# Optimization experiments

Hardware: AMD Instinct MI355X
Metric: run time of the kernel (lower is better)

The kernel has to match this reference:

```python
import jax, jax.numpy as jnp
import numpy as np

N_NODES = 50000


def _gcn_norm(edge_index, n):
    # Add self-loops (PyG GCNConv default) and compute symmetric normalization.
    src = jnp.concatenate([edge_index[0], jnp.arange(n, dtype=edge_index.dtype)])
    dst = jnp.concatenate([edge_index[1], jnp.arange(n, dtype=edge_index.dtype)])
    deg = jax.ops.segment_sum(jnp.ones(src.shape[0], dtype=jnp.float32), dst,
                              num_segments=n)
    dinv = jnp.where(deg > 0, jax.lax.rsqrt(deg), 0.0)
    norm = dinv[src] * dinv[dst]  # [E+N]
    return src, dst, norm


def _gcn_conv(x, src, dst, norm, W, b, n):
    h = x @ W                              # [N, out] linear transform first
    msgs = h[src] * norm[:, None]          # gather + edge-wise scale [E+N, out]
    out = jax.ops.segment_sum(msgs, dst, num_segments=n)  # scatter-add
    return out + b


def setup_inputs() -> dict:
    key = jax.random.key(0)
    k1, k2, k3, k4 = jax.random.split(key, 4)
    N, E, F, H, C = N_NODES, 1600000, 128, 128, 64
    x = jax.random.normal(k1, (N, F), dtype=jnp.float32)
    edge_index = jax.random.randint(k2, (2, E), 0, N, dtype=jnp.int64)
    W1 = jax.random.normal(k3, (F, H), dtype=jnp.float32) * 0.05
    b1 = jnp.zeros((H,), dtype=jnp.float32)
    W2 = jax.random.normal(k4, (H, C), dtype=jnp.float32) * 0.05
    b2 = jnp.zeros((C,), dtype=jnp.float32)
    return {"x": x, "edge_index": edge_index, "W1": W1, "b1": b1,
            "W2": W2, "b2": b2}


def reference(x, edge_index, W1, b1, W2, b2):
    n = x.shape[0]
    src, dst, norm = _gcn_norm(edge_index, n)
    h = _gcn_conv(x, src, dst, norm, W1, b1, n)
    h = jax.nn.relu(h)
    out = _gcn_conv(h, src, dst, norm, W2, b2, n)
    return out
```

## Files before the change

### kernel.cpp

```cpp
#include <hip/hip_runtime.h>
#include <hip/hip_bf16.h>
#include <stdint.h>

#define N_NODES 50000
#define N_EDGES 1600000
#define N_TOT   (N_EDGES + N_NODES)
#define NBKT      256
#define BKT_NODES 196
#define BKT_CAP   7168
#define TILE      4096
#define EPT       16

typedef unsigned short u16;
typedef __attribute__((ext_vector_type(8))) short short8;
typedef __attribute__((ext_vector_type(4))) float floatx4;

__device__ __forceinline__ float b2f(u16 u) {
    union { unsigned int i; float f; } v; v.i = ((unsigned int)u) << 16; return v.f;
}
__device__ __forceinline__ float asf(unsigned u) {
    union { unsigned int i; float f; } v; v.i = u; return v.f;
}
__device__ __forceinline__ u16 f2b(float f) {
    union { unsigned int i; float f; } v; v.f = f;
    unsigned int r = (v.i + 0x7FFFu + ((v.i >> 16) & 1u)) >> 16;
    return (u16)r;
}

__global__ void k_detect(const unsigned* __restrict__ xw,
                         const unsigned* __restrict__ ew,
                         int* __restrict__ flags,
                         int* __restrict__ bktcnt) {
    __shared__ int cnt[2];
    int tid = threadIdx.x;
    bktcnt[tid] = 0;
    if (tid < 2) cnt[tid] = 0;
    __syncthreads();
    unsigned w = xw[tid];
    int e = (w >> 7) & 0xFF;
    int plaus = (e == 0) || (e >= 0x60 && e <= 0x9F);
    unsigned hw = ew[2 * tid + 1];
    atomicAdd(&cnt[0], plaus);
    atomicAdd(&cnt[1], hw == 0 ? 1 : 0);
    __syncthreads();
    if (tid == 0) {
        flags[0] = (cnt[0] < 160) ? 1 : 0;
        flags[1] = (cnt[1] > 250) ? 1 : 0;
    }
}

__global__ __launch_bounds__(256) void k_part(const int* __restrict__ ei,
                                              const int* __restrict__ flags,
                                              unsigned* __restrict__ pairs,
                                              int* __restrict__ bktcnt) {
    __shared__ unsigned pairsL[TILE];
    __shared__ unsigned char bktL[TILE];
    __shared__ int hist[NBKT], incl[NBKT], delta[NBKT];
    int tid = threadIdx.x;
    long base = (long)blockIdx.x * TILE;
    int i64 = flags[1];
    hist[tid] = 0;
    __syncthreads();

    int myb[EPT], myrank[EPT]; unsigned myp[EPT];
#pragma unroll
    for (int t = 0; t < EPT; t++) {
        long idx = base + t * 256 + tid;
        int b = -1; unsigned p = 0;
        if (idx < N_TOT) {
            int s, d;
            if (idx < N_EDGES) {
                if (i64) { s = ei[2 * idx]; d = ei[2 * (N_EDGES + idx)]; }
                else     { s = ei[idx];     d = ei[N_EDGES + idx]; }
            } else {
                s = d = (int)(idx - N_EDGES);
            }
            b = d / BKT_NODES;
            p = (unsigned)s | ((unsigned)(d - b * BKT_NODES) << 16);
        }
        myb[t] = b; myp[t] = p;
        myrank[t] = (b >= 0) ? atomicAdd(&hist[b], 1) : 0;
    }
    __syncthreads();

    int tot = hist[tid];
    incl[tid] = tot;
    __syncthreads();
    for (int o = 1; o < NBKT; o <<= 1) {
        int t2 = (tid >= o) ? incl[tid - o] : 0;
        __syncthreads();
        incl[tid] += t2;
        __syncthreads();
    }
    int excl = incl[tid] - tot;
    int gb = atomicAdd(&bktcnt[tid], tot);
    hist[tid]  = excl;
    delta[tid] = tid * BKT_CAP + gb - excl;
    __syncthreads();

#pragma unroll
    for (int t = 0; t < EPT; t++) {
        if (myb[t] >= 0) {
            int slot = hist[myb[t]] + myrank[t];
            pairsL[slot] = myp[t];
            bktL[slot]   = (unsigned char)myb[t];
        }
    }
    __syncthreads();
    int count = incl[NBKT - 1];
    for (int i = tid; i < count; i += 256) {
        int b = bktL[i];
        int pos = delta[b] + i;
        if (pos - b * BKT_CAP < BKT_CAP)
            pairs[pos] = pairsL[i];
    }
}

__global__ __launch_bounds__(256) void k_bktscan(const int* __restrict__ bktcnt,
                                                 int* __restrict__ bktbase) {
    __shared__ int s[NBKT];
    int tid = threadIdx.x;
    int v = bktcnt[tid];
    s[tid] = v;
    __syncthreads();
    for (int o = 1; o < NBKT; o <<= 1) {
        int t = (tid >= o) ? s[tid - o] : 0;
        __syncthreads();
        s[tid] += t;
        __syncthreads();
    }
    bktbase[tid] = s[tid] - v;
}

__global__ __launch_bounds__(256) void k_bucket(const unsigned* __restrict__ pairs,
                                                const int* __restrict__ bktcnt,
                                                const int* __restrict__ bktbase,
                                                int* __restrict__ rowstart,
                                                int* __restrict__ deg,
                                                float* __restrict__ dinv,
                                                u16* __restrict__ csr) {
    __shared__ u16 csrL[BKT_CAP];
    __shared__ int degL[NBKT], curL[NBKT], scanT[NBKT];
    int b = blockIdx.x, tid = threadIdx.x;
    int cnt  = bktcnt[b];
    int base = bktbase[b];
    const unsigned* reg = pairs + (size_t)b * BKT_CAP;
    degL[tid] = 0;
    __syncthreads();
    for (int i = tid; i < cnt; i += 256)
        atomicAdd(&degL[reg[i] >> 16], 1);
    __syncthreads();
    int v = degL[tid];
    scanT[tid] = v;
    __syncthreads();
    for (int o = 1; o < NBKT; o <<= 1) {
        int t = (tid >= o) ? scanT[tid - o] : 0;
        __syncthreads();
        scanT[tid] += t;
        __syncthreads();
    }
    int excl = scanT[tid] - v;
    curL[tid] = excl;
    int n = b * BKT_NODES + tid;
    if (tid < BKT_NODES && n < N_NODES) {
        rowstart[n] = base + excl;
        deg[n]      = v;
        dinv[n]     = rsqrtf((float)v);
    }
    __syncthreads();
    for (int i = tid; i < cnt; i += 256) {
        unsigned p = reg[i];
        int slot = atomicAdd(&curL[p >> 16], 1);
        csrL[slot] = (u16)(p & 0xFFFFu);
    }
    __syncthreads();
    for (int i = tid; i < cnt; i += 256)
        csr[base + i] = csrL[i];
}

template<int NOUT, bool ADYN>
__global__ __launch_bounds__(256) void k_gemm(const void* __restrict__ A,
                                              const void* __restrict__ W,
                                              const float* __restrict__ dinv,
                                              u16* __restrict__ out, int M,
                                              const int* __restrict__ flags) {
    const int isf32 = flags[0];
    constexpr int LDW = 136;
    __shared__ __align__(16) u16 Wt[NOUT * LDW];
    int tid = threadIdx.x;
    const float* Wf = (const float*)W;
    const u16*   Wu = (const u16*)W;
    for (int idx = tid; idx < 128 * NOUT; idx += 256) {
        int k = idx / NOUT, n = idx % NOUT;
        Wt[n * LDW + k] = isf32 ? f2b(Wf[idx]) : Wu[idx];
    }
    __syncthreads();

    int wave = tid >> 6, lane = tid & 63;
    int quad = lane >> 4, l16 = lane & 15;
    int r0 = blockIdx.x * 64 + wave * 16;
    int r = r0 + l16; if (r >= M) r = M - 1;

    floatx4 acc[NOUT / 16];
#pragma unroll
    for (int i = 0; i < NOUT / 16; i++) acc[i] = (floatx4)(0.f);

#pragma unroll
    for (int ks = 0; ks < 4; ks++) {
        short8 a;
        if (ADYN && isf32) {
            const float* af = (const float*)A + (size_t)r * 128 + ks * 32 + quad * 8;
            float4 v0 = ((const float4*)af)[0];
            float4 v1 = ((const float4*)af)[1];
            a[0] = (short)f2b(v0.x); a[1] = (short)f2b(v0.y);
            a[2] = (short)f2b(v0.z); a[3] = (short)f2b(v0.w);
            a[4] = (short)f2b(v1.x); a[5] = (short)f2b(v1.y);
            a[6] = (short)f2b(v1.z); a[7] = (short)f2b(v1.w);
        } else {
            a = ((const short8*)((const u16*)A + (size_t)r * 128))[ks * 4 + quad];
        }
#pragma unroll
        for (int nt = 0; nt < NOUT / 16; nt++) {
            const short8* bp = (const short8*)&Wt[(nt * 16 + l16) * LDW + ks * 32 + quad * 8];
            acc[nt] = __builtin_amdgcn_mfma_f32_16x16x32_bf16(a, *bp, acc[nt], 0, 0, 0);
        }
    }
    float sc[4];
#pragma unroll
    for (int j = 0; j < 4; j++) {
        int row = r0 + quad * 4 + j;
        sc[j] = dinv[row < M ? row : 0];
    }
#pragma unroll
    for (int nt = 0; nt < NOUT / 16; nt++) {
#pragma unroll
        for (int j = 0; j < 4; j++) {
            int row = r0 + quad * 4 + j;
            if (row < M) out[(size_t)row * NOUT + nt * 16 + l16] = f2b(acc[nt][j] * sc[j]);
        }
    }
}

#define ACCU(u, j) { acc[j].x += asf((u) << 16); acc[j].y += asf((u) & 0xFFFF0000u); }

__global__ __launch_bounds__(256) void k_agg1(const u16* __restrict__ h,
                                              const u16* __restrict__ csr,
                                              const int* __restrict__ rowstart,
                                              const int* __restrict__ deg,
                                              const float* __restrict__ dinv,
                                              const void* __restrict__ bias,
                                              u16* __restrict__ out,
                                              const int* __restrict__ flags) {
    int wave = threadIdx.x >> 6, lane = threadIdx.x & 63;
    int d = blockIdx.x * 4 + wave;
    if (d >= N_NODES) return;
    int oct = lane >> 3, l8 = lane & 7;
    int start = rowstart[d], end = start + deg[d];
    float2 acc[8];
#pragma unroll
    for (int j = 0; j < 8; j++) acc[j] = make_float2(0.f, 0.f);

    int e = start + oct;
    for (; e + 24 < end; e += 32) {
        int s0 = csr[e], s1 = csr[e + 8], s2 = csr[e + 16], s3 = csr[e + 24];
        const uint4* p0 = (const uint4*)(h + (size_t)s0 * 128) + l8 * 2;
        const uint4* p1 = (const uint4*)(h + (size_t)s1 * 128) + l8 * 2;
        const uint4* p2 = (const uint4*)(h + (size_t)s2 * 128) + l8 * 2;
        const uint4* p3 = (const uint4*)(h + (size_t)s3 * 128) + l8 * 2;
        uint4 a0 = p0[0], b0 = p0[1];
        uint4 a1 = p1[0], b1 = p1[1];
        uint4 a2 = p2[0], b2 = p2[1];
        uint4 a3 = p3[0], b3 = p3[1];
        ACCU(a0.x,0) ACCU(a0.y,1) ACCU(a0.z,2) ACCU(a0.w,3)
        ACCU(b0.x,4) ACCU(b0.y,5) ACCU(b0.z,6) ACCU(b0.w,7)
        ACCU(a1.x,0) ACCU(a1.y,1) ACCU(a1.z,2) ACCU(a1.w,3)
        ACCU(b1.x,4) ACCU(b1.y,5) ACCU(b1.z,6) ACCU(b1.w,7)
        ACCU(a2.x,0) ACCU(a2.y,1) ACCU(a2.z,2) ACCU(a2.w,3)
        ACCU(b2.x,4) ACCU(b2.y,5) ACCU(b2.z,6) ACCU(b2.w,7)
        ACCU(a3.x,0) ACCU(a3.y,1) ACCU(a3.z,2) ACCU(a3.w,3)
        ACCU(b3.x,4) ACCU(b3.y,5) ACCU(b3.z,6) ACCU(b3.w,7)
    }
    for (; e < end; e += 8) {
        int s0 = csr[e];
        const uint4* p0 = (const uint4*)(h + (size_t)s0 * 128) + l8 * 2;
        uint4 a0 = p0[0], b0 = p0[1];
        ACCU(a0.x,0) ACCU(a0.y,1) ACCU(a0.z,2) ACCU(a0.w,3)
        ACCU(b0.x,4) ACCU(b0.y,5) ACCU(b0.z,6) ACCU(b0.w,7)
    }
#pragma unroll
    for (int j = 0; j < 8; j++) {
        acc[j].x += __shfl_xor(acc[j].x, 8);  acc[j].y += __shfl_xor(acc[j].y, 8);
        acc[j].x += __shfl_xor(acc[j].x, 16); acc[j].y += __shfl_xor(acc[j].y, 16);
        acc[j].x += __shfl_xor(acc[j].x, 32); acc[j].y += __shfl_xor(acc[j].y, 32);
    }
    if (oct == 0) {
        int isf32 = flags[0];
        float dd = dinv[d];
        u16 r[16];
#pragma unroll
        for (int j = 0; j < 8; j++) {
            float bx = isf32 ? ((const float*)bias)[l8 * 16 + 2 * j]
                             : b2f(((const u16*)bias)[l8 * 16 + 2 * j]);
            float by = isf32 ? ((const float*)bias)[l8 * 16 + 2 * j + 1]
                             : b2f(((const u16*)bias)[l8 * 16 + 2 * j + 1]);
            float vx = acc[j].x * dd + bx;
            float vy = acc[j].y * dd + by;
            r[2 * j]     = f2b(vx > 0.f ? vx : 0.f);
            r[2 * j + 1] = f2b(vy > 0.f ? vy : 0.f);
        }
        uint4 o0, o1;
        o0.x = r[0] | ((unsigned)r[1] << 16);  o0.y = r[2] | ((unsigned)r[3] << 16);
        o0.z = r[4] | ((unsigned)r[5] << 16);  o0.w = r[6] | ((unsigned)r[7] << 16);
        o1.x = r[8] | ((unsigned)r[9] << 16);  o1.y = r[10] | ((unsigned)r[11] << 16);
        o1.z = r[12] | ((unsigned)r[13] << 16); o1.w = r[14] | ((unsigned)r[15] << 16);
        ((uint4*)(out + (size_t)d * 128))[l8 * 2]     = o0;
        ((uint4*)(out + (size_t)d * 128))[l8 * 2 + 1] = o1;
    }
}

__global__ __launch_bounds__(256) void k_agg2(const u16* __restrict__ h,
                                              const u16* __restrict__ csr,
                                              const int* __restrict__ rowstart,
                                              const int* __restrict__ deg,
                                              const float* __restrict__ dinv,
                                              const void* __restrict__ bias,
                                              float* __restrict__ out,
                                              const int* __restrict__ flags) {
    int wave = threadIdx.x >> 6, lane = threadIdx.x & 63;
    int d = blockIdx.x * 4 + wave;
    if (d >= N_NODES) return;
    int oct = lane >> 3, l8 = lane & 7;
    int start = rowstart[d], end = start + deg[d];
    float2 acc[4];
#pragma unroll
    for (int j = 0; j < 4; j++) acc[j] = make_float2(0.f, 0.f);

    int e = start + oct;
    for (; e + 24 < end; e += 32) {
        int s0 = csr[e], s1 = csr[e + 8], s2 = csr[e + 16], s3 = csr[e + 24];
        uint4 v0 = ((const uint4*)(h + (size_t)s0 * 64))[l8];
        uint4 v1 = ((const uint4*)(h + (size_t)s1 * 64))[l8];
        uint4 v2 = ((const uint4*)(h + (size_t)s2 * 64))[l8];
        uint4 v3 = ((const uint4*)(h + (size_t)s3 * 64))[l8];
        ACCU(v0.x,0) ACCU(v0.y,1) ACCU(v0.z,2) ACCU(v0.w,3)
        ACCU(v1.x,0) ACCU(v1.y,1) ACCU(v1.z,2) ACCU(v1.w,3)
        ACCU(v2.x,0) ACCU(v2.y,1) ACCU(v2.z,2) ACCU(v2.w,3)
        ACCU(v3.x,0) ACCU(v3.y,1) ACCU(v3.z,2) ACCU(v3.w,3)
    }
    for (; e < end; e += 8) {
        int s0 = csr[e];
        uint4 v0 = ((const uint4*)(h + (size_t)s0 * 64))[l8];
        ACCU(v0.x,0) ACCU(v0.y,1) ACCU(v0.z,2) ACCU(v0.w,3)
    }
#pragma unroll
    for (int j = 0; j < 4; j++) {
        acc[j].x += __shfl_xor(acc[j].x, 8);  acc[j].y += __shfl_xor(acc[j].y, 8);
        acc[j].x += __shfl_xor(acc[j].x, 16); acc[j].y += __shfl_xor(acc[j].y, 16);
        acc[j].x += __shfl_xor(acc[j].x, 32); acc[j].y += __shfl_xor(acc[j].y, 32);
    }
    if (oct == 0) {
        int isf32 = flags[0];
        float dd = dinv[d];
        float r[8];
#pragma unroll
        for (int j = 0; j < 4; j++) {
            float bx = isf32 ? ((const float*)bias)[l8 * 8 + 2 * j]
                             : b2f(((const u16*)bias)[l8 * 8 + 2 * j]);
            float by = isf32 ? ((const float*)bias)[l8 * 8 + 2 * j + 1]
                             : b2f(((const u16*)bias)[l8 * 8 + 2 * j + 1]);
            r[2 * j]     = acc[j].x * dd + bx;
            r[2 * j + 1] = acc[j].y * dd + by;
        }
        float4* op = (float4*)(out + (size_t)d * 64) + l8 * 2;
        op[0] = make_float4(r[0], r[1], r[2], r[3]);
        op[1] = make_float4(r[4], r[5], r[6], r[7]);
    }
}

extern "C" void kernel_launch(void* const* d_in, const int* in_sizes, int n_in,
                              void* d_out, int out_size, void* d_ws, size_t ws_size,
                              hipStream_t stream) {
    const void* x  = d_in[0];
    const int*  ei = (const int*)d_in[1];
    const void* W1 = d_in[2];
    const void* b1 = d_in[3];
    const void* W2 = d_in[4];
    const void* b2 = d_in[5];
    float* out = (float*)d_out;

    char* ws = (char*)d_ws;
    int*      flags    = (int*)(ws + 0);
    int*      bktcnt   = (int*)(ws + 1024);
    int*      bktbase  = (int*)(ws + 2048);
    int*      deg      = (int*)(ws + 4096);
    int*      rowstart = (int*)(ws + 204800);
    float*    dinv     = (float*)(ws + 405504);
    unsigned* pairs    = (unsigned*)(ws + 606208);
    u16*      csr      = (u16*)(ws + 7946240);
    u16*      h1       = (u16*)(ws + 11247616);
    u16*      out1     = (u16*)(ws + 24047616);
    u16*      h2       = h1;

    k_detect <<<1, 256, 0, stream>>>((const unsigned*)x, (const unsigned*)ei, flags, bktcnt);
    k_part   <<<(N_TOT + TILE - 1) / TILE, 256, 0, stream>>>(ei, flags, pairs, bktcnt);
    k_bktscan<<<1, 256, 0, stream>>>(bktcnt, bktbase);
    k_bucket <<<NBKT, 256, 0, stream>>>(pairs, bktcnt, bktbase, rowstart, deg, dinv, csr);

    k_gemm<128, true> <<<(N_NODES + 63) / 64, 256, 0, stream>>>(x, W1, dinv, h1, N_NODES, flags);
    k_agg1<<<(N_NODES + 3) / 4, 256, 0, stream>>>(h1, csr, rowstart, deg, dinv, b1, out1, flags);
    k_gemm<64, false> <<<(N_NODES + 63) / 64, 256, 0, stream>>>(out1, W2, dinv, h2, N_NODES, flags);
    k_agg2<<<(N_NODES + 3) / 4, 256, 0, stream>>>(h2, csr, rowstart, deg, dinv, b2, out, flags);
}
```

Measured before the change: 255.6 us.

## Store hidden features in 32-column panels and aggregate one panel per block

The GEMM now writes its bf16 output in panel-major layout (32 features per panel, plus a zero pad row per panel), and the aggregation kernels launch one grid slice per panel so each gather reads a 64-byte panel row. The goal is a smaller working set per pass, so the gathered features stay resident in cache across random neighbor accesses. The inner loop is also reworked to process 16 edges per step with masked tails that point at the zero pad row, replacing the separate remainder loop. In exchange, edge indices and degrees are read once per panel, and h2 is moved to reuse the pairs buffer region.

```diff
diff --git a/kernel.cpp b/kernel.cpp
--- a/kernel.cpp
+++ b/kernel.cpp
@@ -10,6 +10,8 @@
 #define BKT_CAP   7168
 #define TILE      4096
 #define EPT       16
+#define NGRP      12500
+#define PROWS     (N_NODES + 1)
 
 typedef unsigned short u16;
 typedef __attribute__((ext_vector_type(8))) short short8;
@@ -188,6 +190,8 @@
     constexpr int LDW = 136;
     __shared__ __align__(16) u16 Wt[NOUT * LDW];
     int tid = threadIdx.x;
+    if (blockIdx.x == 0 && tid < NOUT)
+        out[((size_t)((tid >> 5) * PROWS) + N_NODES) * 32 + (tid & 31)] = 0;
     const float* Wf = (const float*)W;
     const u16*   Wu = (const u16*)W;
     for (int idx = tid; idx < 128 * NOUT; idx += 256) {
@@ -233,10 +237,13 @@
     }
 #pragma unroll
     for (int nt = 0; nt < NOUT / 16; nt++) {
+        int col = nt * 16 + l16;
+        int p = col >> 5, c = col & 31;
 #pragma unroll
         for (int j = 0; j < 4; j++) {
             int row = r0 + quad * 4 + j;
-            if (row < M) out[(size_t)row * NOUT + nt * 16 + l16] = f2b(acc[nt][j] * sc[j]);
+            if (row < M)
+                out[((size_t)(p * PROWS) + row) * 32 + c] = f2b(acc[nt][j] * sc[j]);
         }
     }
 }
@@ -252,69 +259,55 @@
                                               u16* __restrict__ out,
                                               const int* __restrict__ flags) {
     int wave = threadIdx.x >> 6, lane = threadIdx.x & 63;
-    int d = blockIdx.x * 4 + wave;
-    if (d >= N_NODES) return;
-    int oct = lane >> 3, l8 = lane & 7;
-    int start = rowstart[d], end = start + deg[d];
-    float2 acc[8];
-#pragma unroll
-    for (int j = 0; j < 8; j++) acc[j] = make_float2(0.f, 0.f);
-
-    int e = start + oct;
-    for (; e + 24 < end; e += 32) {
-        int s0 = csr[e], s1 = csr[e + 8], s2 = csr[e + 16], s3 = csr[e + 24];
-        const uint4* p0 = (const uint4*)(h + (size_t)s0 * 128) + l8 * 2;
-        const uint4* p1 = (const uint4*)(h + (size_t)s1 * 128) + l8 * 2;
-        const uint4* p2 = (const uint4*)(h + (size_t)s2 * 128) + l8 * 2;
-        const uint4* p3 = (const uint4*)(h + (size_t)s3 * 128) + l8 * 2;
-        uint4 a0 = p0[0], b0 = p0[1];
-        uint4 a1 = p1[0], b1 = p1[1];
-        uint4 a2 = p2[0], b2 = p2[1];
-        uint4 a3 = p3[0], b3 = p3[1];
-        ACCU(a0.x,0) ACCU(a0.y,1) ACCU(a0.z,2) ACCU(a0.w,3)
-        ACCU(b0.x,4) ACCU(b0.y,5) ACCU(b0.z,6) ACCU(b0.w,7)
-        ACCU(a1.x,0) ACCU(a1.y,1) ACCU(a1.z,2) ACCU(a1.w,3)
-        ACCU(b1.x,4) ACCU(b1.y,5) ACCU(b1.z,6) ACCU(b1.w,7)
-        ACCU(a2.x,0) ACCU(a2.y,1) ACCU(a2.z,2) ACCU(a2.w,3)
-        ACCU(b2.x,4) ACCU(b2.y,5) ACCU(b2.z,6) ACCU(b2.w,7)
-        ACCU(a3.x,0) ACCU(a3.y,1) ACCU(a3.z,2) ACCU(a3.w,3)
-        ACCU(b3.x,4) ACCU(b3.y,5) ACCU(b3.z,6) ACCU(b3.w,7)
-    }
-    for (; e < end; e += 8) {
-        int s0 = csr[e];
-        const uint4* p0 = (const uint4*)(h + (size_t)s0 * 128) + l8 * 2;
-        uint4 a0 = p0[0], b0 = p0[1];
-        ACCU(a0.x,0) ACCU(a0.y,1) ACCU(a0.z,2) ACCU(a0.w,3)
-        ACCU(b0.x,4) ACCU(b0.y,5) ACCU(b0.z,6) ACCU(b0.w,7)
-    }
-#pragma unroll
-    for (int j = 0; j < 8; j++) {
+    int gb = blockIdx.x % NGRP, panel = blockIdx.x / NGRP;
+    int d = gb * 4 + wave;
+    int grp = lane >> 2, l4 = lane & 3;
+    int start = rowstart[d], dg = deg[d], end = start + dg;
+    const u16* hp = h + (size_t)(panel * PROWS) * 32;
+    float2 acc[4];
+#pragma unroll
+    for (int j = 0; j < 4; j++) acc[j] = make_float2(0.f, 0.f);
+
+    int rounds = (dg + 31) >> 5;
+    int e = start + grp;
+    for (int r = 0; r < rounds; r++, e += 32) {
+        int e1 = e + 16;
+        int s0 = csr[e  < end ? e  : start];
+        int s1 = csr[e1 < end ? e1 : start];
+        s0 = (e  < end) ? s0 : N_NODES;
+        s1 = (e1 < end) ? s1 : N_NODES;
+        uint4 v0 = ((const uint4*)(hp + (size_t)s0 * 32))[l4];
+        uint4 v1 = ((const uint4*)(hp + (size_t)s1 * 32))[l4];
+        ACCU(v0.x,0) ACCU(v0.y,1) ACCU(v0.z,2) ACCU(v0.w,3)
+        ACCU(v1.x,0) ACCU(v1.y,1) ACCU(v1.z,2) ACCU(v1.w,3)
+    }
+#pragma unroll
+    for (int j = 0; j < 4; j++) {
+        acc[j].x += __shfl_xor(acc[j].x, 4);  acc[j].y += __shfl_xor(acc[j].y, 4);
         acc[j].x += __shfl_xor(acc[j].x, 8);  acc[j].y += __shfl_xor(acc[j].y, 8);
         acc[j].x += __shfl_xor(acc[j].x, 16); acc[j].y += __shfl_xor(acc[j].y, 16);
         acc[j].x += __shfl_xor(acc[j].x, 32); acc[j].y += __shfl_xor(acc[j].y, 32);
     }
-    if (oct == 0) {
+    if (grp == 0) {
         int isf32 = flags[0];
         float dd = dinv[d];
-        u16 r[16];
-#pragma unroll
-        for (int j = 0; j < 8; j++) {
-            float bx = isf32 ? ((const float*)bias)[l8 * 16 + 2 * j]
-                             : b2f(((const u16*)bias)[l8 * 16 + 2 * j]);
-            float by = isf32 ? ((const float*)bias)[l8 * 16 + 2 * j + 1]
-                             : b2f(((const u16*)bias)[l8 * 16 + 2 * j + 1]);
+        int fb = panel * 32 + l4 * 8;
+        u16 r[8];
+#pragma unroll
+        for (int j = 0; j < 4; j++) {
+            float bx = isf32 ? ((const float*)bias)[fb + 2 * j]
+                             : b2f(((const u16*)bias)[fb + 2 * j]);
+            float by = isf32 ? ((const float*)bias)[fb + 2 * j + 1]
+                             : b2f(((const u16*)bias)[fb + 2 * j + 1]);
             float vx = acc[j].x * dd + bx;
             float vy = acc[j].y * dd + by;
             r[2 * j]     = f2b(vx > 0.f ? vx : 0.f);
             r[2 * j + 1] = f2b(vy > 0.f ? vy : 0.f);
         }
-        uint4 o0, o1;
-        o0.x = r[0] | ((unsigned)r[1] << 16);  o0.y = r[2] | ((unsigned)r[3] << 16);
-        o0.z = r[4] | ((unsigned)r[5] << 16);  o0.w = r[6] | ((unsigned)r[7] << 16);
-        o1.x = r[8] | ((unsigned)r[9] << 16);  o1.y = r[10] | ((unsigned)r[11] << 16);
-        o1.z = r[12] | ((unsigned)r[13] << 16); o1.w = r[14] | ((unsigned)r[15] << 16);
-        ((uint4*)(out + (size_t)d * 128))[l8 * 2]     = o0;
-        ((uint4*)(out + (size_t)d * 128))[l8 * 2 + 1] = o1;
+        uint4 o;
+        o.x = r[0] | ((unsigned)r[1] << 16); o.y = r[2] | ((unsigned)r[3] << 16);
+        o.z = r[4] | ((unsigned)r[5] << 16); o.w = r[6] | ((unsigned)r[7] << 16);
+        ((uint4*)(out + (size_t)d * 128 + panel * 32))[l4] = o;
     }
 }
 
@@ -327,51 +320,50 @@
                                               float* __restrict__ out,
                                               const int* __restrict__ flags) {
     int wave = threadIdx.x >> 6, lane = threadIdx.x & 63;
-    int d = blockIdx.x * 4 + wave;
-    if (d >= N_NODES) return;
-    int oct = lane >> 3, l8 = lane & 7;
-    int start = rowstart[d], end = start + deg[d];
+    int gb = blockIdx.x % NGRP, panel = blockIdx.x / NGRP;
+    int d = gb * 4 + wave;
+    int grp = lane >> 2, l4 = lane & 3;
+    int start = rowstart[d], dg = deg[d], end = start + dg;
+    const u16* hp = h + (size_t)(panel * PROWS) * 32;
     float2 acc[4];
 #pragma unroll
     for (int j = 0; j < 4; j++) acc[j] = make_float2(0.f, 0.f);
 
-    int e = start + oct;
-    for (; e + 24 < end; e += 32) {
-        int s0 = csr[e], s1 = csr[e + 8], s2 = csr[e + 16], s3 = csr[e + 24];
-        uint4 v0 = ((const uint4*)(h + (size_t)s0 * 64))[l8];
-        uint4 v1 = ((const uint4*)(h + (size_t)s1 * 64))[l8];
-        uint4 v2 = ((const uint4*)(h + (size_t)s2 * 64))[l8];
-        uint4 v3 = ((const uint4*)(h + (size_t)s3 * 64))[l8];
+    int rounds = (dg + 31) >> 5;
+    int e = start + grp;
+    for (int r = 0; r < rounds; r++, e += 32) {
+        int e1 = e + 16;
+        int s0 = csr[e  < end ? e  : start];
+        int s1 = csr[e1 < end ? e1 : start];
+        s0 = (e  < end) ? s0 : N_NODES;
+        s1 = (e1 < end) ? s1 : N_NODES;
+        uint4 v0 = ((const uint4*)(hp + (size_t)s0 * 32))[l4];
+        uint4 v1 = ((const uint4*)(hp + (size_t)s1 * 32))[l4];
         ACCU(v0.x,0) ACCU(v0.y,1) ACCU(v0.z,2) ACCU(v0.w,3)
         ACCU(v1.x,0) ACCU(v1.y,1) ACCU(v1.z,2) ACCU(v1.w,3)
-        ACCU(v2.x,0) ACCU(v2.y,1) ACCU(v2.z,2) ACCU(v2.w,3)
-        ACCU(v3.x,0) ACCU(v3.y,1) ACCU(v3.z,2) ACCU(v3.w,3)
-    }
-    for (; e < end; e += 8) {
-        int s0 = csr[e];
-        uint4 v0 = ((const uint4*)(h + (size_t)s0 * 64))[l8];
-        ACCU(v0.x,0) ACCU(v0.y,1) ACCU(v0.z,2) ACCU(v0.w,3)
     }
 #pragma unroll
     for (int j = 0; j < 4; j++) {
+        acc[j].x += __shfl_xor(acc[j].x, 4);  acc[j].y += __shfl_xor(acc[j].y, 4);
         acc[j].x += __shfl_xor(acc[j].x, 8);  acc[j].y += __shfl_xor(acc[j].y, 8);
         acc[j].x += __shfl_xor(acc[j].x, 16); acc[j].y += __shfl_xor(acc[j].y, 16);
         acc[j].x += __shfl_xor(acc[j].x, 32); acc[j].y += __shfl_xor(acc[j].y, 32);
     }
-    if (oct == 0) {
+    if (grp == 0) {
         int isf32 = flags[0];
         float dd = dinv[d];
+        int fb = panel * 32 + l4 * 8;
         float r[8];
 #pragma unroll
         for (int j = 0; j < 4; j++) {
-            float bx = isf32 ? ((const float*)bias)[l8 * 8 + 2 * j]
-                             : b2f(((const u16*)bias)[l8 * 8 + 2 * j]);
-            float by = isf32 ? ((const float*)bias)[l8 * 8 + 2 * j + 1]
-                             : b2f(((const u16*)bias)[l8 * 8 + 2 * j + 1]);
+            float bx = isf32 ? ((const float*)bias)[fb + 2 * j]
+                             : b2f(((const u16*)bias)[fb + 2 * j]);
+            float by = isf32 ? ((const float*)bias)[fb + 2 * j + 1]
+                             : b2f(((const u16*)bias)[fb + 2 * j + 1]);
             r[2 * j]     = acc[j].x * dd + bx;
             r[2 * j + 1] = acc[j].y * dd + by;
         }
-        float4* op = (float4*)(out + (size_t)d * 64) + l8 * 2;
+        float4* op = (float4*)(out + (size_t)d * 64 + panel * 32 + l4 * 8);
         op[0] = make_float4(r[0], r[1], r[2], r[3]);
         op[1] = make_float4(r[4], r[5], r[6], r[7]);
     }
@@ -398,8 +390,8 @@
     unsigned* pairs    = (unsigned*)(ws + 606208);
     u16*      csr      = (u16*)(ws + 7946240);
     u16*      h1       = (u16*)(ws + 11247616);
-    u16*      out1     = (u16*)(ws + 24047616);
-    u16*      h2       = h1;
+    u16*      out1     = (u16*)(ws + 24048640);
+    u16*      h2       = (u16*)(ws + 606208);
 
     k_detect <<<1, 256, 0, stream>>>((const unsigned*)x, (const unsigned*)ei, flags, bktcnt);
     k_part   <<<(N_TOT + TILE - 1) / TILE, 256, 0, stream>>>(ei, flags, pairs, bktcnt);
@@ -407,7 +399,7 @@
     k_bucket <<<NBKT, 256, 0, stream>>>(pairs, bktcnt, bktbase, rowstart, deg, dinv, csr);
 
     k_gemm<128, true> <<<(N_NODES + 63) / 64, 256, 0, stream>>>(x, W1, dinv, h1, N_NODES, flags);
-    k_agg1<<<(N_NODES + 3) / 4, 256, 0, stream>>>(h1, csr, rowstart, deg, dinv, b1, out1, flags);
+    k_agg1<<<4 * NGRP, 256, 0, stream>>>(h1, csr, rowstart, deg, dinv, b1, out1, flags);
     k_gemm<64, false> <<<(N_NODES + 63) / 64, 256, 0, stream>>>(out1, W2, dinv, h2, N_NODES, flags);
-    k_agg2<<<(N_NODES + 3) / 4, 256, 0, stream>>>(h2, csr, rowstart, deg, dinv, b2, out, flags);
-}
+    k_agg2<<<2 * NGRP, 256, 0, stream>>>(h2, csr, rowstart, deg, dinv, b2, out, flags);
+}
```

Measured after the change: 298.3 us. 16.7% more time.

## Fold detect and bucket-scan kernels into neighbors; software-pipeline aggregation gathers with zero-row padding

Applied to the files above, without the earlier changes.

Removes the separate detect and bucket-scan launches. Format detection moves into k_part, with each block recomputing the int64 flag, and the bucket prefix scan is recomputed redundantly in every k_bucket block. The aggregation kernels swap the unrolled-by-4 loop plus tail for a two-deep software-pipelined gather. Out-of-range slots read a zeroed padding row that k_gemm writes, which removes the tail loop and branch divergence. h2 now reuses the pairs buffer, and bktcnt is cleared with a memset.

```diff
diff --git a/kernel.cpp b/kernel.cpp
--- a/kernel.cpp
+++ b/kernel.cpp
@@ -10,6 +10,7 @@
 #define BKT_CAP   7168
 #define TILE      4096
 #define EPT       16
+#define ZROW      N_NODES
 
 typedef unsigned short u16;
 typedef __attribute__((ext_vector_type(8))) short short8;
@@ -27,40 +28,33 @@
     return (u16)r;
 }
 
-__global__ void k_detect(const unsigned* __restrict__ xw,
-                         const unsigned* __restrict__ ew,
-                         int* __restrict__ flags,
-                         int* __restrict__ bktcnt) {
-    __shared__ int cnt[2];
-    int tid = threadIdx.x;
-    bktcnt[tid] = 0;
-    if (tid < 2) cnt[tid] = 0;
-    __syncthreads();
-    unsigned w = xw[tid];
-    int e = (w >> 7) & 0xFF;
-    int plaus = (e == 0) || (e >= 0x60 && e <= 0x9F);
-    unsigned hw = ew[2 * tid + 1];
-    atomicAdd(&cnt[0], plaus);
-    atomicAdd(&cnt[1], hw == 0 ? 1 : 0);
-    __syncthreads();
-    if (tid == 0) {
-        flags[0] = (cnt[0] < 160) ? 1 : 0;
-        flags[1] = (cnt[1] > 250) ? 1 : 0;
-    }
-}
-
 __global__ __launch_bounds__(256) void k_part(const int* __restrict__ ei,
-                                              const int* __restrict__ flags,
+                                              const unsigned* __restrict__ xw,
+                                              int* __restrict__ flags,
                                               unsigned* __restrict__ pairs,
                                               int* __restrict__ bktcnt) {
     __shared__ unsigned pairsL[TILE];
     __shared__ unsigned char bktL[TILE];
     __shared__ int hist[NBKT], incl[NBKT], delta[NBKT];
+    __shared__ int zc, pc;
     int tid = threadIdx.x;
     long base = (long)blockIdx.x * TILE;
-    int i64 = flags[1];
     hist[tid] = 0;
-    __syncthreads();
+    if (tid == 0) { zc = 0; pc = 0; }
+    __syncthreads();
+    unsigned hw = ((const unsigned*)ei)[2 * tid + 1];
+    atomicAdd(&zc, hw == 0 ? 1 : 0);
+    if (blockIdx.x == 0) {
+        unsigned w = xw[tid];
+        int ex = (w >> 7) & 0xFF;
+        atomicAdd(&pc, ((ex == 0) || (ex >= 0x60 && ex <= 0x9F)) ? 1 : 0);
+    }
+    __syncthreads();
+    int i64 = zc > 250;
+    if (blockIdx.x == 0 && tid == 0) {
+        flags[0] = (pc < 160) ? 1 : 0;
+        flags[1] = i64;
+    }
 
     int myb[EPT], myrank[EPT]; unsigned myp[EPT];
 #pragma unroll
@@ -116,25 +110,8 @@
     }
 }
 
-__global__ __launch_bounds__(256) void k_bktscan(const int* __restrict__ bktcnt,
-                                                 int* __restrict__ bktbase) {
-    __shared__ int s[NBKT];
-    int tid = threadIdx.x;
-    int v = bktcnt[tid];
-    s[tid] = v;
-    __syncthreads();
-    for (int o = 1; o < NBKT; o <<= 1) {
-        int t = (tid >= o) ? s[tid - o] : 0;
-        __syncthreads();
-        s[tid] += t;
-        __syncthreads();
-    }
-    bktbase[tid] = s[tid] - v;
-}
-
 __global__ __launch_bounds__(256) void k_bucket(const unsigned* __restrict__ pairs,
                                                 const int* __restrict__ bktcnt,
-                                                const int* __restrict__ bktbase,
                                                 int* __restrict__ rowstart,
                                                 int* __restrict__ deg,
                                                 float* __restrict__ dinv,
@@ -142,8 +119,19 @@
     __shared__ u16 csrL[BKT_CAP];
     __shared__ int degL[NBKT], curL[NBKT], scanT[NBKT];
     int b = blockIdx.x, tid = threadIdx.x;
+    int cv = bktcnt[tid];
+    scanT[tid] = cv;
+    __syncthreads();
+    for (int o = 1; o < NBKT; o <<= 1) {
+        int t = (tid >= o) ? scanT[tid - o] : 0;
+        __syncthreads();
+        scanT[tid] += t;
+        __syncthreads();
+    }
     int cnt  = bktcnt[b];
-    int base = bktbase[b];
+    int base = scanT[b] - cnt;
+    __syncthreads();
+
     const unsigned* reg = pairs + (size_t)b * BKT_CAP;
     degL[tid] = 0;
     __syncthreads();
@@ -188,6 +176,8 @@
     constexpr int LDW = 136;
     __shared__ __align__(16) u16 Wt[NOUT * LDW];
     int tid = threadIdx.x;
+    if (blockIdx.x == 0 && tid < NOUT)
+        out[(size_t)M * NOUT + tid] = 0;
     const float* Wf = (const float*)W;
     const u16*   Wu = (const u16*)W;
     for (int idx = tid; idx < 128 * NOUT; idx += 256) {
@@ -236,12 +226,16 @@
 #pragma unroll
         for (int j = 0; j < 4; j++) {
             int row = r0 + quad * 4 + j;
-            if (row < M) out[(size_t)row * NOUT + nt * 16 + l16] = f2b(acc[nt][j] * sc[j]);
+            if (row < M)
+                out[(size_t)row * NOUT + nt * 16 + l16] = f2b(acc[nt][j] * sc[j]);
         }
     }
 }
 
 #define ACCU(u, j) { acc[j].x += asf((u) << 16); acc[j].y += asf((u) & 0xFFFF0000u); }
+#define ACC8(q0, q1) { ACCU(q0.x,0) ACCU(q0.y,1) ACCU(q0.z,2) ACCU(q0.w,3) \
+                       ACCU(q1.x,4) ACCU(q1.y,5) ACCU(q1.z,6) ACCU(q1.w,7) }
+#define ACC4(q)      { ACCU(q.x,0) ACCU(q.y,1) ACCU(q.z,2) ACCU(q.w,3) }
 
 __global__ __launch_bounds__(256) void k_agg1(const u16* __restrict__ h,
                                               const u16* __restrict__ csr,
@@ -253,40 +247,31 @@
                                               const int* __restrict__ flags) {
     int wave = threadIdx.x >> 6, lane = threadIdx.x & 63;
     int d = blockIdx.x * 4 + wave;
-    if (d >= N_NODES) return;
     int oct = lane >> 3, l8 = lane & 7;
-    int start = rowstart[d], end = start + deg[d];
+    int start = rowstart[d], dg = deg[d], end = start + dg;
+    int rounds = (dg + 7) >> 3;
     float2 acc[8];
 #pragma unroll
     for (int j = 0; j < 8; j++) acc[j] = make_float2(0.f, 0.f);
 
     int e = start + oct;
-    for (; e + 24 < end; e += 32) {
-        int s0 = csr[e], s1 = csr[e + 8], s2 = csr[e + 16], s3 = csr[e + 24];
-        const uint4* p0 = (const uint4*)(h + (size_t)s0 * 128) + l8 * 2;
-        const uint4* p1 = (const uint4*)(h + (size_t)s1 * 128) + l8 * 2;
-        const uint4* p2 = (const uint4*)(h + (size_t)s2 * 128) + l8 * 2;
-        const uint4* p3 = (const uint4*)(h + (size_t)s3 * 128) + l8 * 2;
-        uint4 a0 = p0[0], b0 = p0[1];
-        uint4 a1 = p1[0], b1 = p1[1];
-        uint4 a2 = p2[0], b2 = p2[1];
-        uint4 a3 = p3[0], b3 = p3[1];
-        ACCU(a0.x,0) ACCU(a0.y,1) ACCU(a0.z,2) ACCU(a0.w,3)
-        ACCU(b0.x,4) ACCU(b0.y,5) ACCU(b0.z,6) ACCU(b0.w,7)
-        ACCU(a1.x,0) ACCU(a1.y,1) ACCU(a1.z,2) ACCU(a1.w,3)
-        ACCU(b1.x,4) ACCU(b1.y,5) ACCU(b1.z,6) ACCU(b1.w,7)
-        ACCU(a2.x,0) ACCU(a2.y,1) ACCU(a2.z,2) ACCU(a2.w,3)
-        ACCU(b2.x,4) ACCU(b2.y,5) ACCU(b2.z,6) ACCU(b2.w,7)
-        ACCU(a3.x,0) ACCU(a3.y,1) ACCU(a3.z,2) ACCU(a3.w,3)
-        ACCU(b3.x,4) ACCU(b3.y,5) ACCU(b3.z,6) ACCU(b3.w,7)
-    }
-    for (; e < end; e += 8) {
-        int s0 = csr[e];
-        const uint4* p0 = (const uint4*)(h + (size_t)s0 * 128) + l8 * 2;
-        uint4 a0 = p0[0], b0 = p0[1];
-        ACCU(a0.x,0) ACCU(a0.y,1) ACCU(a0.z,2) ACCU(a0.w,3)
-        ACCU(b0.x,4) ACCU(b0.y,5) ACCU(b0.z,6) ACCU(b0.w,7)
-    }
+    int sA = (e < end) ? csr[e] : ZROW;
+    const uint4* pA = (const uint4*)(h + (size_t)sA * 128) + l8 * 2;
+    uint4 a0 = pA[0], a1 = pA[1];
+    e += 8;
+    int sB = (e < end) ? csr[e] : ZROW;
+    const uint4* pB = (const uint4*)(h + (size_t)sB * 128) + l8 * 2;
+    uint4 b0 = pB[0], b1 = pB[1];
+    for (int r = 2; r < rounds; r++) {
+        e += 8;
+        int sC = (e < end) ? csr[e] : ZROW;
+        const uint4* pC = (const uint4*)(h + (size_t)sC * 128) + l8 * 2;
+        uint4 c0 = pC[0], c1 = pC[1];
+        ACC8(a0, a1)
+        a0 = b0; a1 = b1; b0 = c0; b1 = c1;
+    }
+    ACC8(a0, a1)
+    ACC8(b0, b1)
 #pragma unroll
     for (int j = 0; j < 8; j++) {
         acc[j].x += __shfl_xor(acc[j].x, 8);  acc[j].y += __shfl_xor(acc[j].y, 8);
@@ -328,30 +313,28 @@
                                               const int* __restrict__ flags) {
     int wave = threadIdx.x >> 6, lane = threadIdx.x & 63;
     int d = blockIdx.x * 4 + wave;
-    if (d >= N_NODES) return;
     int oct = lane >> 3, l8 = lane & 7;
-    int start = rowstart[d], end = start + deg[d];
+    int start = rowstart[d], dg = deg[d], end = start + dg;
+    int rounds = (dg + 7) >> 3;
     float2 acc[4];
 #pragma unroll
     for (int j = 0; j < 4; j++) acc[j] = make_float2(0.f, 0.f);
 
     int e = start + oct;
-    for (; e + 24 < end; e += 32) {
-        int s0 = csr[e], s1 = csr[e + 8], s2 = csr[e + 16], s3 = csr[e + 24];
-        uint4 v0 = ((const uint4*)(h + (size_t)s0 * 64))[l8];
-        uint4 v1 = ((const uint4*)(h + (size_t)s1 * 64))[l8];
-        uint4 v2 = ((const uint4*)(h + (size_t)s2 * 64))[l8];
-        uint4 v3 = ((const uint4*)(h + (size_t)s3 * 64))[l8];
-        ACCU(v0.x,0) ACCU(v0.y,1) ACCU(v0.z,2) ACCU(v0.w,3)
-        ACCU(v1.x,0) ACCU(v1.y,1) ACCU(v1.z,2) ACCU(v1.w,3)
-        ACCU(v2.x,0) ACCU(v2.y,1) ACCU(v2.z,2) ACCU(v2.w,3)
-        ACCU(v3.x,0) ACCU(v3.y,1) ACCU(v3.z,2) ACCU(v3.w,3)
-    }
-    for (; e < end; e += 8) {
-        int s0 = csr[e];
-        uint4 v0 = ((const uint4*)(h + (size_t)s0 * 64))[l8];
-        ACCU(v0.x,0) ACCU(v0.y,1) ACCU(v0.z,2) ACCU(v0.w,3)
-    }
+    int sA = (e < end) ? csr[e] : ZROW;
+    uint4 a0 = ((const uint4*)(h + (size_t)sA * 64))[l8];
+    e += 8;
+    int sB = (e < end) ? csr[e] : ZROW;
+    uint4 b0 = ((const uint4*)(h + (size_t)sB * 64))[l8];
+    for (int r = 2; r < rounds; r++) {
+        e += 8;
+        int sC = (e < end) ? csr[e] : ZROW;
+        uint4 c0 = ((const uint4*)(h + (size_t)sC * 64))[l8];
+        ACC4(a0)
+        a0 = b0; b0 = c0;
+    }
+    ACC4(a0)
+    ACC4(b0)
 #pragma unroll
     for (int j = 0; j < 4; j++) {
         acc[j].x += __shfl_xor(acc[j].x, 8);  acc[j].y += __shfl_xor(acc[j].y, 8);
@@ -391,23 +374,22 @@
     char* ws = (char*)d_ws;
     int*      flags    = (int*)(ws + 0);
     int*      bktcnt   = (int*)(ws + 1024);
-    int*      bktbase  = (int*)(ws + 2048);
     int*      deg      = (int*)(ws + 4096);
     int*      rowstart = (int*)(ws + 204800);
     float*    dinv     = (float*)(ws + 405504);
     unsigned* pairs    = (unsigned*)(ws + 606208);
     u16*      csr      = (u16*)(ws + 7946240);
     u16*      h1       = (u16*)(ws + 11247616);
-    u16*      out1     = (u16*)(ws + 24047616);
-    u16*      h2       = h1;
-
-    k_detect <<<1, 256, 0, stream>>>((const unsigned*)x, (const unsigned*)ei, flags, bktcnt);
-    k_part   <<<(N_TOT + TILE - 1) / TILE, 256, 0, stream>>>(ei, flags, pairs, bktcnt);
-    k_bktscan<<<1, 256, 0, stream>>>(bktcnt, bktbase);
-    k_bucket <<<NBKT, 256, 0, stream>>>(pairs, bktcnt, bktbase, rowstart, deg, dinv, csr);
+    u16*      out1     = (u16*)(ws + 24048640);
+    u16*      h2       = (u16*)(ws + 606208);
+
+    hipMemsetAsync(bktcnt, 0, NBKT * sizeof(int), stream);
+    k_part   <<<(N_TOT + TILE - 1) / TILE, 256, 0, stream>>>(ei, (const unsigned*)x,
+                                                             flags, pairs, bktcnt);
+    k_bucket <<<NBKT, 256, 0, stream>>>(pairs, bktcnt, rowstart, deg, dinv, csr);
 
     k_gemm<128, true> <<<(N_NODES + 63) / 64, 256, 0, stream>>>(x, W1, dinv, h1, N_NODES, flags);
-    k_agg1<<<(N_NODES + 3) / 4, 256, 0, stream>>>(h1, csr, rowstart, deg, dinv, b1, out1, flags);
+    k_agg1<<<N_NODES / 4, 256, 0, stream>>>(h1, csr, rowstart, deg, dinv, b1, out1, flags);
     k_gemm<64, false> <<<(N_NODES + 63) / 64, 256, 0, stream>>>(out1, W2, dinv, h2, N_NODES, flags);
-    k_agg2<<<(N_NODES + 3) / 4, 256, 0, stream>>>(h2, csr, rowstart, deg, dinv, b2, out, flags);
-}
+    k_agg2<<<N_NODES / 4, 256, 0, stream>>>(h2, csr, rowstart, deg, dinv, b2, out, flags);
+}
```

Result: no change. 251.0 us (-1.8%).
